# Kernel optimization log

Measured on AMD Instinct MI355X. Metric: run time of the kernel, lower is better.

## Reference

```python
import jax, jax.numpy as jnp
import numpy as np

B, T, D, L = 8, 8192, 256, 3
DISTS = (1, 5, 15, 30)


def _layernorm(x, g, b, eps=1e-5):
    m = x.mean(-1, keepdims=True)
    v = ((x - m) ** 2).mean(-1, keepdims=True)
    return (x - m) * jax.lax.rsqrt(v + eps) * g + b


def _temporal_edges():
    src, dst = [], []
    for d in DISTS:
        a = np.arange(T - d)
        src += [a, a + d]
        dst += [a + d, a]
    ei = np.stack([np.concatenate(src), np.concatenate(dst)])  # [2, E]
    off = (np.arange(B) * T).repeat(ei.shape[1])
    return np.tile(ei, (1, B)) + off[None, :]  # [2, B*E]


def setup_inputs() -> dict:
    key = jax.random.key(0)
    ks = jax.random.split(key, 6)
    s = 1.0 / np.sqrt(D)
    s4 = 1.0 / np.sqrt(4 * D)
    return dict(
        x=jax.random.normal(ks[0], (B, T, D), jnp.float32),
        adjacency=jnp.zeros((T, T), jnp.float32),  # shape-check only
        edge_index=jnp.asarray(_temporal_edges(), jnp.int32),
        conv_w=jax.random.normal(ks[1], (L, D, D), jnp.float32) * s,
        conv_b=jnp.zeros((L, D), jnp.float32),
        norm_g=jnp.ones((L, D), jnp.float32),
        norm_b=jnp.zeros((L, D), jnp.float32),
        normff_g=jnp.ones((D,), jnp.float32),
        normff_b=jnp.zeros((D,), jnp.float32),
        w1=jax.random.normal(ks[2], (D, 4 * D), jnp.float32) * s,
        b1=jnp.zeros((4 * D,), jnp.float32),
        w2=jax.random.normal(ks[3], (4 * D, D), jnp.float32) * s4,
        b2=jnp.zeros((D,), jnp.float32),
    )


def reference(x, adjacency, edge_index, conv_w, conv_b, norm_g, norm_b,
              normff_g, normff_b, w1, b1, w2, b2):
    b, t, d = x.shape
    n = b * t
    xf = x.reshape(n, d)
    src, dst = edge_index[0], edge_index[1]
    # GCN symmetric degree normalization (no self loops), degrees by target node
    deg = jax.ops.segment_sum(jnp.ones(src.shape[0], x.dtype), dst, num_segments=n)
    dinv = jnp.where(deg > 0, jax.lax.rsqrt(deg), 0.0)
    enorm = (dinv[src] * dinv[dst])[:, None]  # [E,1]
    for i in range(conv_w.shape[0]):
        h = xf @ conv_w[i]                                    # [N,D]
        h = jax.ops.segment_sum(h[src] * enorm, dst, num_segments=n) + conv_b[i]
        h = jax.nn.gelu(h, approximate=False)
        h = _layernorm(h.reshape(b, t, d), norm_g[i], norm_b[i]).reshape(n, d)
        xf = xf + h
    x = xf.reshape(b, t, d)
    y = _layernorm(x, normff_g, normff_b)
    ff = jax.nn.gelu(y @ w1 + b1, approximate=False) @ w2 + b2
    return x + ff
```

## Files before the change

### kernel.cpp

```cpp
#include <hip/hip_runtime.h>
#include <hip/hip_bf16.h>
#include <math.h>
#include <stdint.h>
#include <stddef.h>

#define TB 8
#define TT 8192
#define DD 256
#define NR (TB * TT)
#define HH 1024
#define LL 3

typedef unsigned short ushort_t;
typedef __attribute__((ext_vector_type(8))) short short8;
typedef __attribute__((ext_vector_type(4))) float floatx4;

__device__ __forceinline__ float bf2f(ushort_t u) {
  union { unsigned int i; float f; } x; x.i = ((unsigned int)u) << 16; return x.f;
}
__device__ __forceinline__ ushort_t f2bf(float f) {
  union { float f; unsigned int i; } x; x.f = f;
  unsigned int r = x.i + 0x7fffu + ((x.i >> 16) & 1u);
  return (ushort_t)(r >> 16);
}
__device__ __forceinline__ float ld_in(const void* p, size_t i, int isf) {
  return isf ? ((const float*)p)[i] : bf2f(((const ushort_t*)p)[i]);
}
__device__ __forceinline__ float gelu_f(float v) {
  const float y = v * (0.7978845608028654f + 0.035677408136300125f * v * v);
  const float e = __expf(-2.0f * y);
  return v * __builtin_amdgcn_rcpf(1.0f + e);
}
__device__ __forceinline__ int deg_of(int t) {
  return (t >= 1) + (t >= 5) + (t >= 15) + (t >= 30)
       + (t < TT - 1) + (t < TT - 5) + (t < TT - 15) + (t < TT - 30);
}

__device__ __forceinline__ void gl_lds16(const ushort_t* g, ushort_t* l) {
  __builtin_amdgcn_global_load_lds(
      (const __attribute__((address_space(1))) unsigned int*)(g),
      (__attribute__((address_space(3))) unsigned int*)(l), 16, 0, 0);
}

__device__ __forceinline__ int xcd_swz(int lin, int nwg) {
  const int q = nwg >> 3;
  return (lin & 7) * q + (lin >> 3);
}

__global__ void k_probe(const void* __restrict__ x, int* __restrict__ flag) {
  if (threadIdx.x == 0 && blockIdx.x == 0) {
    const float* fb = (const float*)x;
    int okf = 0;
    for (int i = 0; i < 128; ++i) {
      const float av = fabsf(fb[i]);
      if (av > 1e-6f && av < 100.f) okf++;
    }
    *flag = (okf >= 115) ? 1 : 0;
  }
}

__global__ __launch_bounds__(256) void k_cvt(const void* __restrict__ x,
                                             ushort_t* __restrict__ xb,
                                             const int* __restrict__ flag) {
  const int isf = *flag;
  const size_t i4 = (size_t)blockIdx.x * 256 + threadIdx.x;
  if (isf) {
    const float4 f = ((const float4*)x)[i4];
    ushort4 u; u.x = f2bf(f.x); u.y = f2bf(f.y); u.z = f2bf(f.z); u.w = f2bf(f.w);
    ((ushort4*)xb)[i4] = u;
  } else {
    ((ushort4*)xb)[i4] = ((const ushort4*)x)[i4];
  }
}

__global__ void k_transpose_all(const void* __restrict__ cw,
                                const void* __restrict__ w1,
                                const void* __restrict__ w2,
                                ushort_t* __restrict__ cwT,
                                ushort_t* __restrict__ w1T,
                                ushort_t* __restrict__ w2T,
                                const int* __restrict__ flag) {
  __shared__ ushort_t tile[32][33];
  const int isf = *flag;
  const int b = blockIdx.x;
  const void* src; ushort_t* dst; int R, C, bx, by; size_t row0;
  if (b < 192) {
    const int i = b >> 6, t = b & 63;
    src = cw; dst = cwT + (size_t)i * DD * DD; row0 = (size_t)i * DD;
    R = DD; C = DD; bx = (t & 7) * 32; by = (t >> 3) * 32;
  } else if (b < 448) {
    const int t = b - 192;
    src = w1; dst = w1T; row0 = 0; R = DD; C = HH;
    bx = (t & 31) * 32; by = (t >> 5) * 32;
  } else {
    const int t = b - 448;
    src = w2; dst = w2T; row0 = 0; R = HH; C = DD;
    bx = (t & 7) * 32; by = (t >> 3) * 32;
  }
  const int tx = threadIdx.x;
  for (int i = threadIdx.y; i < 32; i += 8)
    tile[i][tx] = f2bf(ld_in(src, (row0 + by + i) * (size_t)C + bx + tx, isf));
  __syncthreads();
  for (int i = threadIdx.y; i < 32; i += 8)
    dst[(size_t)(bx + i) * R + by + tx] = tile[tx][i];
}

template <int LNFF>
__global__ __launch_bounds__(256, 2) void k_conv_fused(
    const ushort_t* __restrict__ xin, ushort_t* __restrict__ xout,
    const ushort_t* __restrict__ Bt, const void* __restrict__ bias,
    size_t boff, const void* __restrict__ g, const void* __restrict__ bn,
    size_t goff, const void* __restrict__ gff, const void* __restrict__ bff,
    ushort_t* __restrict__ yout, const int* __restrict__ flag) {
  __shared__ alignas(16) ushort_t smem[35072];
  float* scr      = (float*)smem;
  float* part     = scr;
  float* partsq   = scr + 256;
  float* smu      = scr + 512;
  float* srs      = scr + 576;
  float* gf       = scr + 640;
  float* bf_      = scr + 896;
  ushort_t* aggA  = smem + 2304;
  ushort_t* Bs    = smem + 18688;
  ushort_t* rt    = smem + 2304;
  const int isf = *flag;

  const int tid  = threadIdx.x;
  const int lane = tid & 63;
  const int l16  = lane & 15;
  const int quad = lane >> 4;
  const int w    = tid >> 6;
  const int m0   = xcd_swz(blockIdx.x, gridDim.x) * 64;

  const int rowt = tid >> 3;
  const int segt = tid & 7;
  const ushort_t* pb = Bt + (size_t)rowt * DD + segt * 8;
  ushort_t* lB = Bs + w * 512;
#pragma unroll
  for (int i = 0; i < 8; ++i)
    gl_lds16(pb + (size_t)i * 32 * DD, lB + i * 2048);

  if (LNFF) {
    gf[tid]  = ld_in(gff, tid, isf);
    bf_[tid] = ld_in(bff, tid, isf);
  }

  const int tbase = m0 & (TT - 1);
  const bool interior = (tbase >= 60) && (tbase <= TT - 124);
  const int koffs[8] = {-30, -15, -5, -1, 1, 5, 15, 30};
#pragma unroll
  for (int j = 0; j < 8; ++j) {
    const int id = j * 256 + tid;
    const int r = id >> 5, c = id & 31;
    const ushort_t* base = xin + (size_t)(m0 + r) * DD + c * 8;
    float s[8] = {0.f, 0.f, 0.f, 0.f, 0.f, 0.f, 0.f, 0.f};
    if (interior) {
#pragma unroll
      for (int e = 0; e < 8; ++e) {
        const short8 u = *(const short8*)(base + (ptrdiff_t)koffs[e] * DD);
#pragma unroll
        for (int q2 = 0; q2 < 8; ++q2) s[q2] += bf2f((ushort_t)u[q2]);
      }
#pragma unroll
      for (int q2 = 0; q2 < 8; ++q2) s[q2] *= 0.125f;
    } else {
      const int t = tbase + r;
      const float di = rsqrtf((float)deg_of(t));
#pragma unroll
      for (int e = 0; e < 8; ++e) {
        const int t2 = t + koffs[e];
        if ((unsigned)t2 < (unsigned)TT) {
          const float wgt = di * rsqrtf((float)deg_of(t2));
          const short8 u = *(const short8*)(base + (ptrdiff_t)koffs[e] * DD);
#pragma unroll
          for (int q2 = 0; q2 < 8; ++q2) s[q2] += wgt * bf2f((ushort_t)u[q2]);
        }
      }
    }
    short8 o;
#pragma unroll
    for (int q2 = 0; q2 < 8; ++q2) o[q2] = (short)f2bf(s[q2]);
    *(short8*)(aggA + (c >> 3) * 4096 + r * 64 + (c & 7) * 8) = o;
  }
  __syncthreads();

  floatx4 acc[4][4];
#pragma unroll
  for (int i = 0; i < 4; ++i)
#pragma unroll
    for (int j = 0; j < 4; ++j) acc[i][j] = {0.f, 0.f, 0.f, 0.f};

#pragma unroll
  for (int t = 0; t < 4; ++t) {
    if (t > 0) {
      __syncthreads();
#pragma unroll
      for (int i = 0; i < 8; ++i)
        gl_lds16(pb + t * 64 + (size_t)i * 32 * DD, lB + i * 2048);
      __syncthreads();
    }
    const ushort_t* Ac = aggA + t * 4096;
#pragma unroll
    for (int ks = 0; ks < 2; ++ks) {
      short8 af[4], bfr[4];
#pragma unroll
      for (int mt = 0; mt < 4; ++mt)
        af[mt] = *(const short8*)(Ac + (mt * 16 + l16) * 64 + ks * 32 + quad * 8);
#pragma unroll
      for (int nt = 0; nt < 4; ++nt)
        bfr[nt] = *(const short8*)(Bs + (w * 64 + nt * 16 + l16) * 64 + ks * 32 + quad * 8);
#pragma unroll
      for (int mt = 0; mt < 4; ++mt)
#pragma unroll
        for (int nt = 0; nt < 4; ++nt)
          acc[mt][nt] = __builtin_amdgcn_mfma_f32_16x16x32_bf16(
              af[mt], bfr[nt], acc[mt][nt], 0, 0, 0);
    }
  }

#pragma unroll
  for (int nt = 0; nt < 4; ++nt) {
    const float bv = ld_in(bias, boff + w * 64 + nt * 16 + l16, isf);
#pragma unroll
    for (int mt = 0; mt < 4; ++mt)
#pragma unroll
      for (int r = 0; r < 4; ++r)
        acc[mt][nt][r] = gelu_f(acc[mt][nt][r] + bv);
  }
#pragma unroll
  for (int mt = 0; mt < 4; ++mt) {
#pragma unroll
    for (int r = 0; r < 4; ++r) {
      float p = 0.f, q = 0.f;
#pragma unroll
      for (int nt = 0; nt < 4; ++nt) {
        const float v = acc[mt][nt][r];
        p += v; q += v * v;
      }
#pragma unroll
      for (int o = 8; o > 0; o >>= 1) {
        p += __shfl_xor(p, o, 64);
        q += __shfl_xor(q, o, 64);
      }
      if (l16 == 0) {
        const int rowloc = mt * 16 + quad * 4 + r;
        part[w * 64 + rowloc] = p;
        partsq[w * 64 + rowloc] = q;
      }
    }
  }
  __syncthreads();
  if (tid < 64) {
    const float s  = part[tid] + part[64 + tid] + part[128 + tid] + part[192 + tid];
    const float sq = partsq[tid] + partsq[64 + tid] + partsq[128 + tid] + partsq[192 + tid];
    const float mu = s * (1.0f / DD);
    const float var = sq * (1.0f / DD) - mu * mu;
    smu[tid] = mu;
    srs[tid] = rsqrtf(var + 1e-5f);
  }
  __syncthreads();

#pragma unroll
  for (int nt = 0; nt < 4; ++nt) {
    const int col = w * 64 + nt * 16 + l16;
    const float gv = ld_in(g, goff + col, isf);
    const float bnv = ld_in(bn, goff + col, isf);
#pragma unroll
    for (int mt = 0; mt < 4; ++mt) {
#pragma unroll
      for (int r = 0; r < 4; ++r) {
        const int rowloc = mt * 16 + quad * 4 + r;
        rt[rowloc * 264 + col] =
            f2bf((acc[mt][nt][r] - smu[rowloc]) * srs[rowloc] * gv + bnv);
      }
    }
  }
  __syncthreads();

  float vals[8][8];
  float s_i[8], q_i[8];
#pragma unroll
  for (int i = 0; i < 8; ++i) {
    const int ch = tid + i * 256;
    const int row = ch >> 5, sg = ch & 31;
    const short8 xv = *(const short8*)(xin + (size_t)(m0 + row) * DD + sg * 8);
    const short8 rv = *(const short8*)(rt + row * 264 + sg * 8);
    short8 ov;
    float ps = 0.f, pq = 0.f;
#pragma unroll
    for (int j = 0; j < 8; ++j) {
      const float v = bf2f((ushort_t)xv[j]) + bf2f((ushort_t)rv[j]);
      ov[j] = (short)f2bf(v);
      if (LNFF) { vals[i][j] = v; ps += v; pq += v * v; }
    }
    *(short8*)(xout + (size_t)(m0 + row) * DD + sg * 8) = ov;
    if (LNFF) { s_i[i] = ps; q_i[i] = pq; }
  }
  if (LNFF) {
    const int sg = tid & 31;
#pragma unroll
    for (int i = 0; i < 8; ++i) {
      float a = s_i[i], b = q_i[i];
#pragma unroll
      for (int o = 16; o > 0; o >>= 1) {
        a += __shfl_xor(a, o, 64);
        b += __shfl_xor(b, o, 64);
      }
      const float mu = a * (1.0f / DD);
      const float rs = rsqrtf(b * (1.0f / DD) - mu * mu + 1e-5f);
      const int row = (tid >> 5) + i * 8;
      short8 oy;
#pragma unroll
      for (int j = 0; j < 8; ++j) {
        const int col = sg * 8 + j;
        oy[j] = (short)f2bf((vals[i][j] - mu) * rs * gf[col] + bf_[col]);
      }
      *(short8*)(yout + (size_t)(m0 + row) * DD + sg * 8) = oy;
    }
  }
}

template <int EPI, int NNT, int KK>
__global__ __launch_bounds__(256, 2) void k_gemm(
    const ushort_t* __restrict__ A, const ushort_t* __restrict__ Bt,
    void* C, size_t coff, const void* __restrict__ bias, size_t boff,
    const ushort_t* __restrict__ resid, const int* __restrict__ flag) {
  __shared__ alignas(16) ushort_t smem[32768];
  const int isf = *flag;
  constexpr int NN = NNT * 128;

  const int tid  = threadIdx.x;
  const int lane = tid & 63;
  const int l16  = lane & 15;
  const int quad = lane >> 4;
  const int wave = tid >> 6;
  const int wm = wave >> 1, wn = wave & 1;
  const int w_ = xcd_swz(blockIdx.x, gridDim.x);
  const int m0 = (w_ / NNT) * 128;
  const int n0 = (w_ % NNT) * 128;

  floatx4 acc[4][4];
#pragma unroll
  for (int i = 0; i < 4; ++i)
#pragma unroll
    for (int j = 0; j < 4; ++j) acc[i][j] = {0.f, 0.f, 0.f, 0.f};

  const int rowt = tid >> 3;
  const int segt = tid & 7;
  const ushort_t* pa = A  + (size_t)(m0 + rowt) * KK + segt * 8;
  const ushort_t* pb = Bt + (size_t)(n0 + rowt) * KK + segt * 8;

  auto stage = [&](int b, int k0) {
    ushort_t* lA = smem + b * 8192 + wave * 512;
    ushort_t* lB = smem + 16384 + b * 8192 + wave * 512;
#pragma unroll
    for (int i = 0; i < 4; ++i) {
      gl_lds16(pa + k0 + (size_t)i * 32 * KK, lA + i * 2048);
      gl_lds16(pb + k0 + (size_t)i * 32 * KK, lB + i * 2048);
    }
  };

  constexpr int NT = KK / 64;
  stage(0, 0);

  for (int t = 0; t < NT; ++t) {
    const int cur = t & 1;
    if (t + 1 < NT) {
      stage(cur ^ 1, (t + 1) * 64);
      asm volatile("s_waitcnt vmcnt(8)" ::: "memory");
    } else {
      asm volatile("s_waitcnt vmcnt(0)" ::: "memory");
    }
    __builtin_amdgcn_s_barrier();
    __builtin_amdgcn_sched_barrier(0);

    const ushort_t* Ac = smem + cur * 8192;
    const ushort_t* Bc = smem + 16384 + cur * 8192;
#pragma unroll
    for (int ks = 0; ks < 2; ++ks) {
      short8 af[4], bfr[4];
#pragma unroll
      for (int mt = 0; mt < 4; ++mt)
        af[mt] = *(const short8*)(Ac + (wm * 64 + mt * 16 + l16) * 64 + ks * 32 + quad * 8);
#pragma unroll
      for (int nt = 0; nt < 4; ++nt)
        bfr[nt] = *(const short8*)(Bc + (wn * 64 + nt * 16 + l16) * 64 + ks * 32 + quad * 8);
#pragma unroll
      for (int mt = 0; mt < 4; ++mt)
#pragma unroll
        for (int nt = 0; nt < 4; ++nt)
          acc[mt][nt] = __builtin_amdgcn_mfma_f32_16x16x32_bf16(
              af[mt], bfr[nt], acc[mt][nt], 0, 0, 0);
    }

    asm volatile("" ::: "memory");
    __builtin_amdgcn_sched_barrier(0);
    __builtin_amdgcn_s_barrier();
  }

  if (EPI == 1) {
    ushort_t* ct = smem;
#pragma unroll
    for (int nt = 0; nt < 4; ++nt) {
      const int lc = wn * 64 + nt * 16 + l16;
      const float bv = ld_in(bias, boff + n0 + lc, isf);
#pragma unroll
      for (int mt = 0; mt < 4; ++mt)
#pragma unroll
        for (int r = 0; r < 4; ++r) {
          const int lr = wm * 64 + mt * 16 + quad * 4 + r;
          ct[lr * 136 + lc] = f2bf(gelu_f(acc[mt][nt][r] + bv));
        }
    }
    __syncthreads();
    const int r0 = tid >> 4;
    const int c0 = (tid & 15) * 8;
#pragma unroll
    for (int i = 0; i < 8; ++i) {
      const int row = r0 + i * 16;
      const short8 v = *(const short8*)(ct + row * 136 + c0);
      *(short8*)((ushort_t*)C + (size_t)(m0 + row) * NN + n0 + c0) = v;
    }
  } else {
#pragma unroll
    for (int i = 0; i < 8; ++i) {
      const int ch = wave * 64 + lane + i * 256;
      const int rr_ = ch >> 4, sg = ch & 15;
      gl_lds16(resid + (size_t)(m0 + rr_) * NN + n0 + sg * 8,
               smem + (size_t)(wave * 64 + i * 256) * 8);
    }
    __syncthreads();
#pragma unroll
    for (int nt = 0; nt < 4; ++nt) {
      const int lc = wn * 64 + nt * 16 + l16;
      const float bv = ld_in(bias, boff + n0 + lc, isf);
#pragma unroll
      for (int mt = 0; mt < 4; ++mt) {
#pragma unroll
        for (int r = 0; r < 4; ++r) {
          const int lr = wm * 64 + mt * 16 + quad * 4 + r;
          const float v = acc[mt][nt][r] + bv + bf2f(smem[lr * 128 + lc]);
          const size_t idx = (size_t)(m0 + lr) * NN + n0 + lc;
          if (isf) ((float*)C)[coff + idx] = v;
          else     ((ushort_t*)C)[coff + idx] = f2bf(v);
        }
      }
    }
  }
}

extern "C" void kernel_launch(void* const* d_in, const int* in_sizes, int n_in,
                              void* d_out, int out_size, void* d_ws, size_t ws_size,
                              hipStream_t stream) {
  const void* x      = d_in[0];
  const void* conv_w = d_in[3];
  const void* conv_b = d_in[4];
  const void* norm_g = d_in[5];
  const void* norm_b = d_in[6];
  const void* nff_g  = d_in[7];
  const void* nff_b  = d_in[8];
  const void* w1     = d_in[9];
  const void* b1     = d_in[10];
  const void* w2     = d_in[11];
  const void* b2     = d_in[12];
  (void)in_sizes; (void)n_in; (void)out_size;

  char* ws = (char*)d_ws;
  int*      flag = (int*)ws;      ws += 16;
  ushort_t* xA   = (ushort_t*)ws; ws += (size_t)NR * DD * 2;
  ushort_t* xB   = (ushort_t*)ws; ws += (size_t)NR * DD * 2;
  ushort_t* yB   = (ushort_t*)ws; ws += (size_t)NR * DD * 2;
  ushort_t* cwT  = (ushort_t*)ws; ws += (size_t)LL * DD * DD * 2;
  ushort_t* w1T  = (ushort_t*)ws; ws += (size_t)DD * HH * 2;
  ushort_t* w2T  = (ushort_t*)ws; ws += (size_t)HH * DD * 2;
  ushort_t* zc   = (ushort_t*)ws;
  const size_t fixed = (size_t)(ws - (char*)d_ws);
  int nch = 1;
  while (nch < 64 && fixed + ((size_t)NR / nch) * HH * 2 > ws_size) nch *= 2;
  const int rchunk = NR / nch;

  k_probe<<<1, 64, 0, stream>>>(x, flag);
  k_transpose_all<<<704, dim3(32, 8), 0, stream>>>(
      conv_w, w1, w2, cwT, w1T, w2T, flag);
  k_cvt<<<(NR * DD / 4) / 256, 256, 0, stream>>>(x, xA, flag);

  k_conv_fused<0><<<NR / 64, 256, 0, stream>>>(
      xA, xB, cwT, conv_b, 0, norm_g, norm_b, 0,
      nullptr, nullptr, nullptr, flag);
  k_conv_fused<0><<<NR / 64, 256, 0, stream>>>(
      xB, xA, cwT + (size_t)DD * DD, conv_b, DD, norm_g, norm_b, DD,
      nullptr, nullptr, nullptr, flag);
  k_conv_fused<1><<<NR / 64, 256, 0, stream>>>(
      xA, xB, cwT + (size_t)2 * DD * DD, conv_b, 2 * DD, norm_g, norm_b,
      2 * DD, nff_g, nff_b, yB, flag);

  for (int c = 0; c < nch; ++c) {
    const size_t ro = (size_t)c * rchunk;
    k_gemm<1, 8, DD><<<(rchunk / 128) * 8, 256, 0, stream>>>(
        yB + ro * DD, w1T, zc, 0, b1, 0, nullptr, flag);
    k_gemm<2, 2, HH><<<(rchunk / 128) * 2, 256, 0, stream>>>(
        zc, w2T, d_out, ro * DD, b2, 0, xB + ro * DD, flag);
  }
}
```

Before: 710.9 us.

## Fuse FFN layernorm, both GEMMs, GELU and residual into one kernel

Replaces the two separate FFN GEMM launches and the layernorm-in-conv epilogue with a single k_ffn kernel. Each 128-row tile is normalized into LDS, and the 1024-wide hidden activation is produced in 128-column chunks and consumed immediately by the second GEMM, so it never goes to global memory. This removes the hidden-tensor and y-tensor round trips. The cost is that weight tiles are single-buffered with a barrier around every load, with no prefetch overlap, and 128KB of LDS per block limits occupancy.

```diff
diff --git a/kernel.cpp b/kernel.cpp
--- a/kernel.cpp
+++ b/kernel.cpp
@@ -105,21 +105,17 @@
     dst[(size_t)(bx + i) * R + by + tx] = tile[tx][i];
 }
 
-template <int LNFF>
 __global__ __launch_bounds__(256, 2) void k_conv_fused(
     const ushort_t* __restrict__ xin, ushort_t* __restrict__ xout,
     const ushort_t* __restrict__ Bt, const void* __restrict__ bias,
     size_t boff, const void* __restrict__ g, const void* __restrict__ bn,
-    size_t goff, const void* __restrict__ gff, const void* __restrict__ bff,
-    ushort_t* __restrict__ yout, const int* __restrict__ flag) {
+    size_t goff, const int* __restrict__ flag) {
   __shared__ alignas(16) ushort_t smem[35072];
   float* scr      = (float*)smem;
   float* part     = scr;
   float* partsq   = scr + 256;
   float* smu      = scr + 512;
   float* srs      = scr + 576;
-  float* gf       = scr + 640;
-  float* bf_      = scr + 896;
   ushort_t* aggA  = smem + 2304;
   ushort_t* Bs    = smem + 18688;
   ushort_t* rt    = smem + 2304;
@@ -139,11 +135,6 @@
 #pragma unroll
   for (int i = 0; i < 8; ++i)
     gl_lds16(pb + (size_t)i * 32 * DD, lB + i * 2048);
-
-  if (LNFF) {
-    gf[tid]  = ld_in(gff, tid, isf);
-    bf_[tid] = ld_in(bff, tid, isf);
-  }
 
   const int tbase = m0 & (TT - 1);
   const bool interior = (tbase >= 60) && (tbase <= TT - 124);
@@ -277,8 +268,6 @@
   }
   __syncthreads();
 
-  float vals[8][8];
-  float s_i[8], q_i[8];
 #pragma unroll
   for (int i = 0; i < 8; ++i) {
     const int ch = tid + i * 256;
@@ -286,164 +275,175 @@
     const short8 xv = *(const short8*)(xin + (size_t)(m0 + row) * DD + sg * 8);
     const short8 rv = *(const short8*)(rt + row * 264 + sg * 8);
     short8 ov;
-    float ps = 0.f, pq = 0.f;
-#pragma unroll
-    for (int j = 0; j < 8; ++j) {
-      const float v = bf2f((ushort_t)xv[j]) + bf2f((ushort_t)rv[j]);
-      ov[j] = (short)f2bf(v);
-      if (LNFF) { vals[i][j] = v; ps += v; pq += v * v; }
-    }
+#pragma unroll
+    for (int j = 0; j < 8; ++j)
+      ov[j] = (short)f2bf(bf2f((ushort_t)xv[j]) + bf2f((ushort_t)rv[j]));
     *(short8*)(xout + (size_t)(m0 + row) * DD + sg * 8) = ov;
-    if (LNFF) { s_i[i] = ps; q_i[i] = pq; }
-  }
-  if (LNFF) {
-    const int sg = tid & 31;
-#pragma unroll
-    for (int i = 0; i < 8; ++i) {
-      float a = s_i[i], b = q_i[i];
-#pragma unroll
-      for (int o = 16; o > 0; o >>= 1) {
-        a += __shfl_xor(a, o, 64);
-        b += __shfl_xor(b, o, 64);
-      }
-      const float mu = a * (1.0f / DD);
-      const float rs = rsqrtf(b * (1.0f / DD) - mu * mu + 1e-5f);
-      const int row = (tid >> 5) + i * 8;
-      short8 oy;
-#pragma unroll
-      for (int j = 0; j < 8; ++j) {
-        const int col = sg * 8 + j;
-        oy[j] = (short)f2bf((vals[i][j] - mu) * rs * gf[col] + bf_[col]);
-      }
-      *(short8*)(yout + (size_t)(m0 + row) * DD + sg * 8) = oy;
-    }
-  }
-}
-
-template <int EPI, int NNT, int KK>
-__global__ __launch_bounds__(256, 2) void k_gemm(
-    const ushort_t* __restrict__ A, const ushort_t* __restrict__ Bt,
-    void* C, size_t coff, const void* __restrict__ bias, size_t boff,
-    const ushort_t* __restrict__ resid, const int* __restrict__ flag) {
-  __shared__ alignas(16) ushort_t smem[32768];
+  }
+}
+
+__global__ __launch_bounds__(512, 2) void k_ffn(
+    const ushort_t* __restrict__ xb, const ushort_t* __restrict__ w1T,
+    const ushort_t* __restrict__ w2T, const void* __restrict__ gff,
+    const void* __restrict__ bff, const void* __restrict__ b1,
+    const void* __restrict__ b2, void* __restrict__ dout,
+    const int* __restrict__ flag) {
+  __shared__ alignas(16) ushort_t smem[65536];
+  ushort_t* An = smem;
+  ushort_t* Zs = smem + 32768;
+  ushort_t* Bs = smem + 49152;
+  ushort_t* Rs = smem + 32768;
   const int isf = *flag;
-  constexpr int NN = NNT * 128;
 
   const int tid  = threadIdx.x;
   const int lane = tid & 63;
   const int l16  = lane & 15;
   const int quad = lane >> 4;
-  const int wave = tid >> 6;
-  const int wm = wave >> 1, wn = wave & 1;
-  const int w_ = xcd_swz(blockIdx.x, gridDim.x);
-  const int m0 = (w_ / NNT) * 128;
-  const int n0 = (w_ % NNT) * 128;
-
-  floatx4 acc[4][4];
+  const int W    = tid >> 6;
+  const int wr   = W >> 2;
+  const int wc   = W & 3;
+  const int m0   = xcd_swz(blockIdx.x, gridDim.x) * 128;
+
+  const int sg = tid & 31;
+  float gffv[8], bffv[8];
+#pragma unroll
+  for (int j = 0; j < 8; ++j) {
+    gffv[j] = ld_in(gff, sg * 8 + j, isf);
+    bffv[j] = ld_in(bff, sg * 8 + j, isf);
+  }
+#pragma unroll
+  for (int i = 0; i < 8; ++i) {
+    const int row = (tid + i * 512) >> 5;
+    const short8 xv = *(const short8*)(xb + (size_t)(m0 + row) * DD + sg * 8);
+    float v[8], ps = 0.f, pq = 0.f;
+#pragma unroll
+    for (int j = 0; j < 8; ++j) {
+      v[j] = bf2f((ushort_t)xv[j]); ps += v[j]; pq += v[j] * v[j];
+    }
+#pragma unroll
+    for (int o = 16; o > 0; o >>= 1) {
+      ps += __shfl_xor(ps, o, 64);
+      pq += __shfl_xor(pq, o, 64);
+    }
+    const float mu = ps * (1.0f / DD);
+    const float rs = rsqrtf(pq * (1.0f / DD) - mu * mu + 1e-5f);
+    short8 o8;
+#pragma unroll
+    for (int j = 0; j < 8; ++j)
+      o8[j] = (short)f2bf((v[j] - mu) * rs * gffv[j] + bffv[j]);
+    *(short8*)(An + (sg >> 3) * 8192 + row * 64 + (sg & 7) * 8) = o8;
+  }
+
+  floatx4 acc2[4][4];
 #pragma unroll
   for (int i = 0; i < 4; ++i)
 #pragma unroll
-    for (int j = 0; j < 4; ++j) acc[i][j] = {0.f, 0.f, 0.f, 0.f};
+    for (int j = 0; j < 4; ++j) acc2[i][j] = {0.f, 0.f, 0.f, 0.f};
 
   const int rowt = tid >> 3;
   const int segt = tid & 7;
-  const ushort_t* pa = A  + (size_t)(m0 + rowt) * KK + segt * 8;
-  const ushort_t* pb = Bt + (size_t)(n0 + rowt) * KK + segt * 8;
-
-  auto stage = [&](int b, int k0) {
-    ushort_t* lA = smem + b * 8192 + wave * 512;
-    ushort_t* lB = smem + 16384 + b * 8192 + wave * 512;
-#pragma unroll
-    for (int i = 0; i < 4; ++i) {
-      gl_lds16(pa + k0 + (size_t)i * 32 * KK, lA + i * 2048);
-      gl_lds16(pb + k0 + (size_t)i * 32 * KK, lB + i * 2048);
-    }
-  };
-
-  constexpr int NT = KK / 64;
-  stage(0, 0);
-
-  for (int t = 0; t < NT; ++t) {
-    const int cur = t & 1;
-    if (t + 1 < NT) {
-      stage(cur ^ 1, (t + 1) * 64);
-      asm volatile("s_waitcnt vmcnt(8)" ::: "memory");
-    } else {
-      asm volatile("s_waitcnt vmcnt(0)" ::: "memory");
-    }
-    __builtin_amdgcn_s_barrier();
-    __builtin_amdgcn_sched_barrier(0);
-
-    const ushort_t* Ac = smem + cur * 8192;
-    const ushort_t* Bc = smem + 16384 + cur * 8192;
-#pragma unroll
-    for (int ks = 0; ks < 2; ++ks) {
-      short8 af[4], bfr[4];
+  ushort_t* lB = Bs + W * 512;
+
+  __syncthreads();
+
+  for (int n1 = 0; n1 < 8; ++n1) {
+    floatx4 acc1[4][2];
+#pragma unroll
+    for (int i = 0; i < 4; ++i)
+#pragma unroll
+      for (int j = 0; j < 2; ++j) acc1[i][j] = {0.f, 0.f, 0.f, 0.f};
+
+#pragma unroll
+    for (int kc = 0; kc < 4; ++kc) {
+      __syncthreads();
+#pragma unroll
+      for (int i = 0; i < 2; ++i)
+        gl_lds16(w1T + (size_t)(n1 * 128 + i * 64 + rowt) * DD + kc * 64 + segt * 8,
+                 lB + i * 4096);
+      __syncthreads();
+#pragma unroll
+      for (int ks = 0; ks < 2; ++ks) {
+        short8 af[4], bfr[2];
+#pragma unroll
+        for (int mt = 0; mt < 4; ++mt)
+          af[mt] = *(const short8*)(An + kc * 8192 +
+                      (wr * 64 + mt * 16 + l16) * 64 + ks * 32 + quad * 8);
+#pragma unroll
+        for (int nt = 0; nt < 2; ++nt)
+          bfr[nt] = *(const short8*)(Bs +
+                      (wc * 32 + nt * 16 + l16) * 64 + ks * 32 + quad * 8);
+#pragma unroll
+        for (int mt = 0; mt < 4; ++mt)
+#pragma unroll
+          for (int nt = 0; nt < 2; ++nt)
+            acc1[mt][nt] = __builtin_amdgcn_mfma_f32_16x16x32_bf16(
+                af[mt], bfr[nt], acc1[mt][nt], 0, 0, 0);
+      }
+    }
+
+#pragma unroll
+    for (int nt = 0; nt < 2; ++nt) {
+      const int col = wc * 32 + nt * 16 + l16;
+      const float b1v = ld_in(b1, n1 * 128 + col, isf);
 #pragma unroll
       for (int mt = 0; mt < 4; ++mt)
-        af[mt] = *(const short8*)(Ac + (wm * 64 + mt * 16 + l16) * 64 + ks * 32 + quad * 8);
-#pragma unroll
-      for (int nt = 0; nt < 4; ++nt)
-        bfr[nt] = *(const short8*)(Bc + (wn * 64 + nt * 16 + l16) * 64 + ks * 32 + quad * 8);
-#pragma unroll
-      for (int mt = 0; mt < 4; ++mt)
+#pragma unroll
+        for (int r = 0; r < 4; ++r) {
+          const int row = wr * 64 + mt * 16 + quad * 4 + r;
+          Zs[(col >> 6) * 8192 + row * 64 + (col & 63)] =
+              f2bf(gelu_f(acc1[mt][nt][r] + b1v));
+        }
+    }
+
+#pragma unroll
+    for (int kc2 = 0; kc2 < 2; ++kc2) {
+      __syncthreads();
+#pragma unroll
+      for (int i = 0; i < 4; ++i)
+        gl_lds16(w2T + (size_t)(i * 64 + rowt) * HH + n1 * 128 + kc2 * 64 + segt * 8,
+                 lB + i * 4096);
+      __syncthreads();
+#pragma unroll
+      for (int ks = 0; ks < 2; ++ks) {
+        short8 af[4], bfr[4];
+#pragma unroll
+        for (int mt = 0; mt < 4; ++mt)
+          af[mt] = *(const short8*)(Zs + kc2 * 8192 +
+                      (wr * 64 + mt * 16 + l16) * 64 + ks * 32 + quad * 8);
 #pragma unroll
         for (int nt = 0; nt < 4; ++nt)
-          acc[mt][nt] = __builtin_amdgcn_mfma_f32_16x16x32_bf16(
-              af[mt], bfr[nt], acc[mt][nt], 0, 0, 0);
-    }
-
-    asm volatile("" ::: "memory");
-    __builtin_amdgcn_sched_barrier(0);
-    __builtin_amdgcn_s_barrier();
-  }
-
-  if (EPI == 1) {
-    ushort_t* ct = smem;
-#pragma unroll
-    for (int nt = 0; nt < 4; ++nt) {
-      const int lc = wn * 64 + nt * 16 + l16;
-      const float bv = ld_in(bias, boff + n0 + lc, isf);
-#pragma unroll
-      for (int mt = 0; mt < 4; ++mt)
-#pragma unroll
-        for (int r = 0; r < 4; ++r) {
-          const int lr = wm * 64 + mt * 16 + quad * 4 + r;
-          ct[lr * 136 + lc] = f2bf(gelu_f(acc[mt][nt][r] + bv));
-        }
-    }
-    __syncthreads();
-    const int r0 = tid >> 4;
-    const int c0 = (tid & 15) * 8;
-#pragma unroll
-    for (int i = 0; i < 8; ++i) {
-      const int row = r0 + i * 16;
-      const short8 v = *(const short8*)(ct + row * 136 + c0);
-      *(short8*)((ushort_t*)C + (size_t)(m0 + row) * NN + n0 + c0) = v;
-    }
-  } else {
-#pragma unroll
-    for (int i = 0; i < 8; ++i) {
-      const int ch = wave * 64 + lane + i * 256;
-      const int rr_ = ch >> 4, sg = ch & 15;
-      gl_lds16(resid + (size_t)(m0 + rr_) * NN + n0 + sg * 8,
-               smem + (size_t)(wave * 64 + i * 256) * 8);
-    }
-    __syncthreads();
-#pragma unroll
-    for (int nt = 0; nt < 4; ++nt) {
-      const int lc = wn * 64 + nt * 16 + l16;
-      const float bv = ld_in(bias, boff + n0 + lc, isf);
-#pragma unroll
-      for (int mt = 0; mt < 4; ++mt) {
-#pragma unroll
-        for (int r = 0; r < 4; ++r) {
-          const int lr = wm * 64 + mt * 16 + quad * 4 + r;
-          const float v = acc[mt][nt][r] + bv + bf2f(smem[lr * 128 + lc]);
-          const size_t idx = (size_t)(m0 + lr) * NN + n0 + lc;
-          if (isf) ((float*)C)[coff + idx] = v;
-          else     ((ushort_t*)C)[coff + idx] = f2bf(v);
-        }
+          bfr[nt] = *(const short8*)(Bs +
+                      (wc * 64 + nt * 16 + l16) * 64 + ks * 32 + quad * 8);
+#pragma unroll
+        for (int mt = 0; mt < 4; ++mt)
+#pragma unroll
+          for (int nt = 0; nt < 4; ++nt)
+            acc2[mt][nt] = __builtin_amdgcn_mfma_f32_16x16x32_bf16(
+                af[mt], bfr[nt], acc2[mt][nt], 0, 0, 0);
+      }
+    }
+  }
+
+  __syncthreads();
+#pragma unroll
+  for (int i = 0; i < 8; ++i)
+    gl_lds16(xb + (size_t)(m0 + i * 16 + (tid >> 5)) * DD + (tid & 31) * 8,
+             Rs + i * 4096 + W * 512);
+  __syncthreads();
+
+#pragma unroll
+  for (int nt = 0; nt < 4; ++nt) {
+    const int col = wc * 64 + nt * 16 + l16;
+    const float b2v = ld_in(b2, col, isf);
+#pragma unroll
+    for (int mt = 0; mt < 4; ++mt) {
+#pragma unroll
+      for (int r = 0; r < 4; ++r) {
+        const int lr = wr * 64 + mt * 16 + quad * 4 + r;
+        const float v = acc2[mt][nt][r] + b2v + bf2f(Rs[lr * 256 + col]);
+        const size_t idx = (size_t)(m0 + lr) * DD + col;
+        if (isf) ((float*)dout)[idx] = v;
+        else     ((ushort_t*)dout)[idx] = f2bf(v);
       }
     }
   }
@@ -463,42 +463,29 @@
   const void* b1     = d_in[10];
   const void* w2     = d_in[11];
   const void* b2     = d_in[12];
-  (void)in_sizes; (void)n_in; (void)out_size;
+  (void)in_sizes; (void)n_in; (void)out_size; (void)ws_size;
 
   char* ws = (char*)d_ws;
   int*      flag = (int*)ws;      ws += 16;
   ushort_t* xA   = (ushort_t*)ws; ws += (size_t)NR * DD * 2;
   ushort_t* xB   = (ushort_t*)ws; ws += (size_t)NR * DD * 2;
-  ushort_t* yB   = (ushort_t*)ws; ws += (size_t)NR * DD * 2;
   ushort_t* cwT  = (ushort_t*)ws; ws += (size_t)LL * DD * DD * 2;
   ushort_t* w1T  = (ushort_t*)ws; ws += (size_t)DD * HH * 2;
   ushort_t* w2T  = (ushort_t*)ws; ws += (size_t)HH * DD * 2;
-  ushort_t* zc   = (ushort_t*)ws;
-  const size_t fixed = (size_t)(ws - (char*)d_ws);
-  int nch = 1;
-  while (nch < 64 && fixed + ((size_t)NR / nch) * HH * 2 > ws_size) nch *= 2;
-  const int rchunk = NR / nch;
 
   k_probe<<<1, 64, 0, stream>>>(x, flag);
   k_transpose_all<<<704, dim3(32, 8), 0, stream>>>(
       conv_w, w1, w2, cwT, w1T, w2T, flag);
   k_cvt<<<(NR * DD / 4) / 256, 256, 0, stream>>>(x, xA, flag);
 
-  k_conv_fused<0><<<NR / 64, 256, 0, stream>>>(
-      xA, xB, cwT, conv_b, 0, norm_g, norm_b, 0,
-      nullptr, nullptr, nullptr, flag);
-  k_conv_fused<0><<<NR / 64, 256, 0, stream>>>(
-      xB, xA, cwT + (size_t)DD * DD, conv_b, DD, norm_g, norm_b, DD,
-      nullptr, nullptr, nullptr, flag);
-  k_conv_fused<1><<<NR / 64, 256, 0, stream>>>(
+  k_conv_fused<<<NR / 64, 256, 0, stream>>>(
+      xA, xB, cwT, conv_b, 0, norm_g, norm_b, 0, flag);
+  k_conv_fused<<<NR / 64, 256, 0, stream>>>(
+      xB, xA, cwT + (size_t)DD * DD, conv_b, DD, norm_g, norm_b, DD, flag);
+  k_conv_fused<<<NR / 64, 256, 0, stream>>>(
       xA, xB, cwT + (size_t)2 * DD * DD, conv_b, 2 * DD, norm_g, norm_b,
-      2 * DD, nff_g, nff_b, yB, flag);
-
-  for (int c = 0; c < nch; ++c) {
-    const size_t ro = (size_t)c * rchunk;
-    k_gemm<1, 8, DD><<<(rchunk / 128) * 8, 256, 0, stream>>>(
-        yB + ro * DD, w1T, zc, 0, b1, 0, nullptr, flag);
-    k_gemm<2, 2, HH><<<(rchunk / 128) * 2, 256, 0, stream>>>(
-        zc, w2T, d_out, ro * DD, b2, 0, xB + ro * DD, flag);
-  }
-}
+      2 * DD, flag);
+
+  k_ffn<<<NR / 128, 512, 0, stream>>>(
+      xB, w1T, w2T, nff_g, nff_b, b1, b2, d_out, flag);
+}
```

New measurement: 712.4 us. About the same (+0.2%).
